# Optimization experiments

Measured on AMD Instinct MI355X. Metric: run time of the kernel, lower is better.

## Reference

```python
import jax, jax.numpy as jnp
import numpy as np
from jax import lax

B, C_IN, T = 64, 40, 8192

def conv1d(x, w, b):
    # x: [B,C,T], w: [O,I,K] (torch Conv1d layout), stride 2, VALID padding
    y = lax.conv_general_dilated(x, w, window_strides=(2,), padding='VALID',
                                 dimension_numbers=('NCH', 'OIH', 'NCH'))
    return y + b[None, :, None]

def avgpool2(x):
    # AvgPool1d(kernel=2, stride=2): pairwise mean, drop trailing odd element
    t2 = x.shape[-1] // 2
    return x[..., :2 * t2].reshape(x.shape[0], x.shape[1], t2, 2).mean(-1)

def setup_inputs():
    key = jax.random.key(0)
    ks = jax.random.split(key, 24)
    def w_init(k, shape, fan_in):
        return jax.random.normal(k, shape, jnp.float32) * (1.0 / np.sqrt(fan_in))
    inp = {}
    inp['x_input'] = jax.random.normal(ks[0], (B, C_IN, T), jnp.float32)
    # per-sample valid lengths in [2048, 8192] so the deep strided stack leaves >=1 frame
    inp['len_mask'] = 2048 + jax.random.randint(ks[1], (B,), 0, T - 2048 + 1, dtype=jnp.int32)
    convs = [(96, C_IN, 10), (96, 96, 5), (96, 96, 5), (96, 96, 5), (96, 96, 5), (96, 96, 5), (128, 96, 3)]
    for i, (o, ci, k) in enumerate(convs):
        inp[f'w{i+1}'] = w_init(ks[2 + 2 * i], (o, ci, k), ci * k)
        inp[f'b{i+1}'] = jnp.zeros((o,), jnp.float32)
    lins = [(128, 128), (64, 128), (5, 64)]
    for i, (o, ci) in enumerate(lins):
        inp[f'lw{i+1}'] = w_init(ks[16 + 2 * i], (o, ci), ci)
        inp[f'lb{i+1}'] = jnp.zeros((o,), jnp.float32)
    return inp

def reference(x_input, len_mask, w1, b1, w2, b2, w3, b3, w4, b4, w5, b5, w6, b6, w7, b7,
              lw1, lb1, lw2, lb2, lw3, lb3):
    # Batched masked equivalent of the per-sample ragged loop: for VALID stride-2 convs,
    # output position j depends only on inputs < valid length when j < valid out-length,
    # so we run batched convs on padded input and track per-sample valid lengths.
    Lv = len_mask.astype(jnp.int32)
    x = jax.nn.relu(conv1d(x_input, w1, b1)); Lv = (Lv - 10) // 2 + 1
    x = jax.nn.relu(conv1d(x, w2, b2));       Lv = (Lv - 5) // 2 + 1
    x = jax.nn.relu(conv1d(x, w3, b3));       Lv = (Lv - 5) // 2 + 1
    # cnn_1d_top (dropout in eval mode = identity)
    x = conv1d(x, w4, b4);        Lv = (Lv - 5) // 2 + 1
    x = jax.nn.relu(avgpool2(x)); Lv = Lv // 2
    x = conv1d(x, w5, b5);        Lv = (Lv - 5) // 2 + 1
    x = jax.nn.relu(avgpool2(x)); Lv = Lv // 2
    x = jax.nn.relu(conv1d(x, w6, b6)); Lv = (Lv - 5) // 2 + 1
    x = jax.nn.relu(conv1d(x, w7, b7)); Lv = (Lv - 3) // 2 + 1
    # AdaptiveMaxPool1d(1) over each sample's valid region
    mask = jnp.arange(x.shape[-1])[None, :] < Lv[:, None]          # [B, T_out]
    x = jnp.max(jnp.where(mask[:, None, :], x, -jnp.inf), axis=-1)  # [B, 128]
    # out1_top MLP head
    h = jax.nn.relu(x @ lw1.T + lb1)
    h = jax.nn.relu(h @ lw2.T + lb2)
    return h @ lw3.T + lb3
```

## Files before the change

### kernel.cpp

```cpp
#include <hip/hip_runtime.h>
#include <hip/hip_bf16.h>
#include <math.h>


typedef __attribute__((ext_vector_type(8))) _Float16 f16x8;
typedef __attribute__((ext_vector_type(4))) float f32x4;

__device__ __forceinline__ unsigned short f2h_bits(float f) {
    union { _Float16 h; unsigned short u; } cv;
    cv.h = (_Float16)f;
    return cv.u;
}

template<int KEFF, int CI, int NBLK, bool IN_FP32, bool RELU, bool OUT_F16, bool POOL>
__global__ __launch_bounds__(512, 2)
void conv_nb(const unsigned short* __restrict__ xh,
             const unsigned short* __restrict__ wpk,
             const float* __restrict__ bias,
             unsigned short* __restrict__ yh,
             float* __restrict__ yf,
             int Tin, int Tout)
{
    constexpr int CO    = 96;
    constexpr int NTHR  = 512;
    constexpr int GTOT  = CI * KEFF;
    constexpr int STEPS = (GTOT + 31) / 32;
    constexpr int RD    = NBLK + KEFF / 2;
    constexpr int NTW   = NBLK / 64;
    constexpr int TOT   = CI * RD;
    constexpr int NIT   = (TOT + NTHR - 1) / NTHR;
    constexpr int PH    = (32 % KEFF == 0) ? 1 : 5;
    constexpr int PERRD = (32 * PH / KEFF) * RD;

    __shared__ unsigned int Bs[TOT];

    const int tid  = threadIdx.x;
    const int lane = tid & 63;
    const int wave = tid >> 6;
    const int mg   = wave & 1;
    const int tg   = wave >> 1;
    const int quad = lane >> 4;
    const int l16  = lane & 15;
    const int wc0  = tg * (NBLK / 4);

    const int nT = (Tout + NBLK - 1) / NBLK;
    const int b  = blockIdx.x / nT;
    const int t0 = (blockIdx.x % nT) * NBLK;

    const float* xf = (const float*)xh;
    const unsigned int* xb = (const unsigned int*)xh + (((size_t)b * CI * Tin) >> 1);
    const int rowd = Tin >> 1;

    #pragma unroll
    for (int it = 0; it < NIT; ++it) {
        int i = tid + it * NTHR;
        if (i < TOT) {
            int r = (unsigned)i / (unsigned)RD, d = i - r * RD;
            unsigned int v;
            if (IN_FP32) {
                int e = 2 * (t0 + d);
                if (e > Tin - 2) e = Tin - 2;
                const float* src = xf + ((size_t)b * CI + r) * Tin + e;
                float2 w = *(const float2*)src;
                v = (unsigned int)f2h_bits(w.x) | ((unsigned int)f2h_bits(w.y) << 16);
            } else {
                int dd = t0 + d;
                if (dd > rowd - 1) dd = rowd - 1;
                v = *(xb + (size_t)r * rowd + dd);
            }
            Bs[i] = v;
        }
    }
    __syncthreads();

    int offb[PH][4];
    #pragma unroll
    for (int ph = 0; ph < PH; ++ph)
        #pragma unroll
        for (int p = 0; p < 4; ++p) {
            int g = 32 * ph + quad * 8 + 2 * p;
            unsigned ci = (unsigned)g / (unsigned)KEFF;
            unsigned dwo = ((unsigned)g - ci * (unsigned)KEFF) >> 1;
            offb[ph][p] = (int)ci * RD + wc0 + l16 + (int)dwo;
        }

    f32x4 acc[3][NTW];
    #pragma unroll
    for (int mt = 0; mt < 3; ++mt)
        #pragma unroll
        for (int nt = 0; nt < NTW; ++nt) acc[mt][nt] = (f32x4)0.f;

    #pragma unroll
    for (int s = 0; s < STEPS; ++s) {
        union BvU { unsigned int u[4]; f16x8 v; } Bv[NTW];
        if (32 * (s + 1) <= GTOT) {
            #pragma unroll
            for (int nt = 0; nt < NTW; ++nt)
                #pragma unroll
                for (int p = 0; p < 4; ++p)
                    Bv[nt].u[p] = Bs[offb[s % PH][p] + (s / PH) * PERRD + nt * 16];
        } else {
            #pragma unroll
            for (int nt = 0; nt < NTW; ++nt)
                #pragma unroll
                for (int p = 0; p < 4; ++p) {
                    int g = 32 * s + quad * 8 + 2 * p;
                    if (g > GTOT - 2) g = GTOT - 2;
                    unsigned ci = (unsigned)g / (unsigned)KEFF;
                    unsigned dwo = ((unsigned)g - ci * (unsigned)KEFF) >> 1;
                    Bv[nt].u[p] = Bs[(int)ci * RD + wc0 + l16 + (int)dwo + nt * 16];
                }
        }

        const unsigned short* ap = wpk + (size_t)s * 6144 + (size_t)(mg * 3) * 512
                                 + (size_t)lane * 8;
        f16x8 Ah[3], Al[3];
        #pragma unroll
        for (int mt = 0; mt < 3; ++mt) {
            Ah[mt] = *(const f16x8*)(ap + mt * 512);
            Al[mt] = *(const f16x8*)(ap + 3072 + mt * 512);
        }
        #pragma unroll
        for (int mt = 0; mt < 3; ++mt)
            #pragma unroll
            for (int nt = 0; nt < NTW; ++nt)
                acc[mt][nt] = __builtin_amdgcn_mfma_f32_16x16x32_f16(Ah[mt], Bv[nt].v, acc[mt][nt], 0, 0, 0);
        #pragma unroll
        for (int mt = 0; mt < 3; ++mt)
            #pragma unroll
            for (int nt = 0; nt < NTW; ++nt)
                acc[mt][nt] = __builtin_amdgcn_mfma_f32_16x16x32_f16(Al[mt], Bv[nt].v, acc[mt][nt], 0, 0, 0);
    }

    #pragma unroll
    for (int mt = 0; mt < 3; ++mt) {
        #pragma unroll
        for (int r = 0; r < 4; ++r) {
            int o = (mg * 3 + mt) * 16 + quad * 4 + r;
            float bv = bias[o];
            #pragma unroll
            for (int nt = 0; nt < NTW; ++nt) {
                int t = t0 + wc0 + nt * 16 + l16;
                float v = acc[mt][nt][r] + bv;
                if (RELU) v = fmaxf(v, 0.f);
                if (POOL) {
                    float sum = v + __shfl_xor(v, 1, 64);
                    if ((lane & 1) == 0 && t + 1 < Tout) {
                        float pr = fmaxf(0.5f * sum, 0.f);
                        size_t pidx = ((size_t)b * CO + o) * (Tout >> 1) + (t >> 1);
                        if (OUT_F16) yh[pidx] = f2h_bits(pr);
                        else         yf[pidx] = pr;
                    }
                } else if (t < Tout) {
                    size_t oidx = ((size_t)b * CO + o) * Tout + t;
                    if (OUT_F16) yh[oidx] = f2h_bits(v);
                    else         yf[oidx] = v;
                }
            }
        }
    }
}

__device__ __forceinline__ void repack_img(const float* __restrict__ w,
                                           unsigned short* __restrict__ wpk,
                                           int idx, int KP, int KW, int CI)
{
    int j = idx & 7, lane = (idx >> 3) & 63, g = idx >> 9;
    int c = g / 24, r = g % 24;
    int mt = r % 6, sh = r / 6;
    int half = sh & 1, s = sh >> 1;
    int S  = c * 2 + s;
    int kg = S * 32 + (lane >> 4) * 8 + j;
    int o  = mt * 16 + (lane & 15);
    int ci = kg / KP, k = kg - ci * KP;
    float val = (ci < CI && k < KW) ? w[((size_t)o * CI + ci) * KW + k] : 0.f;
    _Float16 hh = (_Float16)val;
    union { _Float16 h; unsigned short u; } cv;
    cv.h = (half == 0) ? hh : (_Float16)(val - (float)hh);
    wpk[idx] = cv.u;
}
__device__ __forceinline__ void repack_okc(const float* __restrict__ w,
                                           float* __restrict__ wr,
                                           int idx, int CI, int K, int CO)
{
    int o = idx % CO; int rem = idx / CO; int k = rem % K; int ci = rem / K;
    wr[idx] = w[((size_t)o * CI + ci) * K + k];
}

__global__ void repack_all(const float* w1, const float* w2, const float* w3,
                           const float* w4, const float* w5, const float* w6,
                           const float* w7,
                           unsigned short* p1, unsigned short* p2,
                           unsigned short* p3, unsigned short* p4,
                           unsigned short* p5, float* r6, float* r7)
{
    int idx = blockIdx.x * 256 + threadIdx.x;
    if (idx < 79872)  { repack_img(w1, p1, idx, 10, 10, 40); return; }
    idx -= 79872;
    if (idx < 147456) { repack_img(w2, p2, idx, 8, 5, 96); return; }
    idx -= 147456;
    if (idx < 147456) { repack_img(w3, p3, idx, 8, 5, 96); return; }
    idx -= 147456;
    if (idx < 147456) { repack_img(w4, p4, idx, 8, 5, 96); return; }
    idx -= 147456;
    if (idx < 147456) { repack_img(w5, p5, idx, 8, 5, 96); return; }
    idx -= 147456;
    if (idx < 46080)  { repack_okc(w6, r6, idx, 96, 5, 96); return; }
    idx -= 46080;
    if (idx < 36864)  { repack_okc(w7, r7, idx, 96, 3, 128); return; }
}

__global__ __launch_bounds__(256)
void conv6_k(const float* __restrict__ y5p, const float* __restrict__ w6r,
             const float* __restrict__ b6, float* __restrict__ y6)
{
    __shared__ float s5[96 * 62];
    const int b = blockIdx.x >> 2, ob = blockIdx.x & 3;
    const int tid = threadIdx.x;
    for (int i = tid; i < 96 * 62; i += 256) s5[i] = y5p[(size_t)b * 96 * 62 + i];
    __syncthreads();

    const int wave = __builtin_amdgcn_readfirstlane(tid >> 6);
    const int t = tid & 63;
    if (t < 29) {
        const int o0 = ob * 24 + wave * 6;
        float a[6];
        #pragma unroll
        for (int oo = 0; oo < 6; oo++) a[oo] = 0.f;
        for (int ci = 0; ci < 96; ci++) {
            float xr[5];
            #pragma unroll
            for (int k = 0; k < 5; k++) xr[k] = s5[ci * 62 + 2 * t + k];
            #pragma unroll
            for (int k = 0; k < 5; k++) {
                const float* wp = w6r + (ci * 5 + k) * 96 + o0;
                #pragma unroll
                for (int oo = 0; oo < 6; oo++)
                    a[oo] = fmaf(wp[oo], xr[k], a[oo]);
            }
        }
        #pragma unroll
        for (int oo = 0; oo < 6; oo++)
            y6[((size_t)b * 96 + o0 + oo) * 29 + t] = fmaxf(a[oo] + b6[o0 + oo], 0.f);
    }
}

__global__ __launch_bounds__(256)
void tail2(const float* __restrict__ y6,
           const float* __restrict__ w7r, const float* __restrict__ b7,
           const int* __restrict__ lens,
           const float* __restrict__ lw1, const float* __restrict__ lb1,
           const float* __restrict__ lw2, const float* __restrict__ lb2,
           const float* __restrict__ lw3, const float* __restrict__ lb3,
           float* __restrict__ out)
{
    __shared__ float s6[96 * 29 + 8];
    __shared__ float s7[128 * 14];
    __shared__ float feat[128], h1[128], h2[64];

    const int b = blockIdx.x, tid = threadIdx.x;
    for (int i = tid; i < 96 * 29; i += 256) s6[i] = y6[(size_t)b * 96 * 29 + i];
    __syncthreads();

    const int wave = __builtin_amdgcn_readfirstlane(tid >> 6);
    const int lane = tid & 63;
    const int sub  = lane >> 4;
    const int tl   = lane & 15;
    {
        float a[32];
        #pragma unroll
        for (int oo = 0; oo < 32; oo++) a[oo] = 0.f;
        const int ci0 = sub * 24;
        for (int ci = ci0; ci < ci0 + 24; ci++) {
            float xr[3];
            #pragma unroll
            for (int k = 0; k < 3; k++) xr[k] = s6[ci * 29 + 2 * tl + k];
            #pragma unroll
            for (int k = 0; k < 3; k++) {
                const float* wp = w7r + (ci * 3 + k) * 128 + wave * 32;
                #pragma unroll
                for (int oo = 0; oo < 32; oo++)
                    a[oo] = fmaf(wp[oo], xr[k], a[oo]);
            }
        }
        #pragma unroll
        for (int oo = 0; oo < 32; oo++) {
            float v = a[oo];
            v += __shfl_xor(v, 16, 64);
            v += __shfl_xor(v, 32, 64);
            if (sub == 0 && tl < 14) {
                int o = wave * 32 + oo;
                s7[o * 14 + tl] = fmaxf(v + b7[o], 0.f);
            }
        }
    }
    __syncthreads();

    if (tid < 128) {
        int L = lens[b];
        L = (L - 10) / 2 + 1;
        L = (L - 5) / 2 + 1;
        L = (L - 5) / 2 + 1;
        L = (L - 5) / 2 + 1;
        L = L / 2;
        L = (L - 5) / 2 + 1;
        L = L / 2;
        L = (L - 5) / 2 + 1;
        L = (L - 3) / 2 + 1;
        float m = -INFINITY;
        for (int t = 0; t < L; t++) m = fmaxf(m, s7[tid * 14 + t]);
        feat[tid] = m;
    }
    __syncthreads();

    if (tid < 128) {
        float s = lb1[tid];
        for (int i = 0; i < 128; i++) s = fmaf(lw1[tid * 128 + i], feat[i], s);
        h1[tid] = fmaxf(s, 0.f);
    }
    __syncthreads();
    if (tid < 64) {
        float s = lb2[tid];
        for (int i = 0; i < 128; i++) s = fmaf(lw2[tid * 128 + i], h1[i], s);
        h2[tid] = fmaxf(s, 0.f);
    }
    __syncthreads();
    if (tid < 5) {
        float s = lb3[tid];
        for (int i = 0; i < 64; i++) s = fmaf(lw3[tid * 64 + i], h2[i], s);
        out[b * 5 + tid] = s;
    }
}

extern "C" void kernel_launch(void* const* d_in, const int* in_sizes, int n_in,
                              void* d_out, int out_size, void* d_ws, size_t ws_size,
                              hipStream_t stream)
{
    const float* x    = (const float*)d_in[0];
    const int*   lens = (const int*)  d_in[1];
    const float* w1 = (const float*)d_in[2];   const float* b1 = (const float*)d_in[3];
    const float* w2 = (const float*)d_in[4];   const float* b2 = (const float*)d_in[5];
    const float* w3 = (const float*)d_in[6];   const float* b3 = (const float*)d_in[7];
    const float* w4 = (const float*)d_in[8];   const float* b4 = (const float*)d_in[9];
    const float* w5 = (const float*)d_in[10];  const float* b5 = (const float*)d_in[11];
    const float* w6 = (const float*)d_in[12];  const float* b6 = (const float*)d_in[13];
    const float* w7 = (const float*)d_in[14];  const float* b7 = (const float*)d_in[15];
    const float* lw1 = (const float*)d_in[16]; const float* lb1 = (const float*)d_in[17];
    const float* lw2 = (const float*)d_in[18]; const float* lb2 = (const float*)d_in[19];
    const float* lw3 = (const float*)d_in[20]; const float* lb3 = (const float*)d_in[21];
    float* out = (float*)d_out;
    char*  W   = (char*)d_ws;

    size_t off = 0;
    auto take = [&](size_t bytes) {
        size_t o = off; off = (off + bytes + 255) & ~(size_t)255; return o;
    };
    size_t o_y3h = take(((size_t)64 * 96 * 1020 + 2048) * 2);
    size_t o_y4h = take(((size_t)64 * 96 * 254 + 2048) * 2);
    size_t o_y5p = take((size_t)64 * 96 * 62 * 4 + 1024);
    size_t o_y6  = take((size_t)64 * 96 * 29 * 4);
    size_t o_wp1 = take((size_t)79872 * 2);
    size_t o_wp2 = take((size_t)147456 * 2);
    size_t o_wp3 = take((size_t)147456 * 2);
    size_t o_wp4 = take((size_t)147456 * 2);
    size_t o_wp5 = take((size_t)147456 * 2);
    size_t o_w6r = take((size_t)46080 * 4);
    size_t o_w7r = take((size_t)36864 * 4);
    size_t persist = off;

    auto chunk_bytes = [&](int Bc) -> size_t {
        size_t s = 0;
        s += ((size_t)Bc * 96 * 4092 + 2048) * 2 + 256;
        s += ((size_t)Bc * 96 * 2044 + 2048) * 2 + 256;
        return s;
    };
    int Bc = 64;
    while (Bc > 1 && persist + chunk_bytes(Bc) > ws_size) Bc >>= 1;
    size_t o_y1h = take(((size_t)Bc * 96 * 4092 + 2048) * 2);
    size_t o_y2h = take(((size_t)Bc * 96 * 2044 + 2048) * 2);

    auto US = [&](size_t o) { return (unsigned short*)(W + o); };
    auto FP = [&](size_t o) { return (float*)(W + o); };

    repack_all<<<dim3((752640 + 255) / 256), 256, 0, stream>>>(
        w1, w2, w3, w4, w5, w6, w7,
        US(o_wp1), US(o_wp2), US(o_wp3), US(o_wp4), US(o_wp5),
        FP(o_w6r), FP(o_w7r));

    const int nchunks = 64 / Bc;
    for (int c = 0; c < nchunks; c++) {
        const float* xc = x + (size_t)c * Bc * 40 * 8192;

        conv_nb<10, 40, 256, true, true, true, false><<<dim3(Bc * 16), 512, 0, stream>>>(
            (const unsigned short*)xc, US(o_wp1), b1, US(o_y1h), nullptr, 8192, 4092);
        conv_nb< 8, 96, 128, false, true, true, false><<<dim3(Bc * 16), 512, 0, stream>>>(
            US(o_y1h), US(o_wp2), b2, US(o_y2h), nullptr, 4092, 2044);
        unsigned short* y3h_c = US(o_y3h) + (size_t)c * Bc * 96 * 1020;
        conv_nb< 8, 96, 128, false, true, true, false><<<dim3(Bc * 8), 512, 0, stream>>>(
            US(o_y2h), US(o_wp3), b3, y3h_c, nullptr, 2044, 1020);
    }

    conv_nb<8, 96, 64, false, false, true, true><<<dim3(64 * 8), 512, 0, stream>>>(
        US(o_y3h), US(o_wp4), b4, US(o_y4h), nullptr, 1020, 508);

    conv_nb<8, 96, 64, false, false, false, true><<<dim3(64 * 2), 512, 0, stream>>>(
        US(o_y4h), US(o_wp5), b5, nullptr, FP(o_y5p), 254, 125);

    conv6_k<<<dim3(256), 256, 0, stream>>>(FP(o_y5p), FP(o_w6r), b6, FP(o_y6));

    tail2<<<dim3(64), 256, 0, stream>>>(
        FP(o_y6), FP(o_w7r), b7, lens, lw1, lb1, lw2, lb2, lw3, lb3, out);
}
```

Baseline: 414.1 us.

## Shrink K=5 conv padding to 6, double-buffer MFMA operands, pack f16 stores

The K=5 convolutions now pad the effective kernel to 6 taps instead of 8. This cuts the reduction depth, and with it the MFMA steps and the packed-weight size, by a quarter. A new phase count of 3 handles the new stride. The main loop now prefetches the next step's LDS and weight operands into alternate registers, with sched barriers and setprio around the MFMA block. Non-pooled f16 outputs are paired through a lane shuffle and written as 32-bit stores. Risks are higher register pressure from double buffering, and a possibly dropped last element when Tout is odd in the paired store.

New measurement: 395.9 us. 1.05x faster.

```diff
diff --git a/kernel.cpp b/kernel.cpp
--- a/kernel.cpp
+++ b/kernel.cpp
@@ -29,7 +29,7 @@
     constexpr int NTW   = NBLK / 64;
     constexpr int TOT   = CI * RD;
     constexpr int NIT   = (TOT + NTHR - 1) / NTHR;
-    constexpr int PH    = (32 % KEFF == 0) ? 1 : 5;
+    constexpr int PH    = (32 % KEFF == 0) ? 1 : (((32 * 3) % KEFF == 0) ? 3 : 5);
     constexpr int PERRD = (32 * PH / KEFF) * RD;
 
     __shared__ unsigned int Bs[TOT];
@@ -90,9 +90,9 @@
         #pragma unroll
         for (int nt = 0; nt < NTW; ++nt) acc[mt][nt] = (f32x4)0.f;
 
-    #pragma unroll
-    for (int s = 0; s < STEPS; ++s) {
-        union BvU { unsigned int u[4]; f16x8 v; } Bv[NTW];
+    union BvU { unsigned int u[4]; f16x8 v; };
+
+    auto load_step = [&](int s, BvU (&Bv)[NTW], f16x8 (&Ah)[3], f16x8 (&Al)[3]) {
         if (32 * (s + 1) <= GTOT) {
             #pragma unroll
             for (int nt = 0; nt < NTW; ++nt)
@@ -111,15 +111,15 @@
                     Bv[nt].u[p] = Bs[(int)ci * RD + wc0 + l16 + (int)dwo + nt * 16];
                 }
         }
-
         const unsigned short* ap = wpk + (size_t)s * 6144 + (size_t)(mg * 3) * 512
                                  + (size_t)lane * 8;
-        f16x8 Ah[3], Al[3];
         #pragma unroll
         for (int mt = 0; mt < 3; ++mt) {
             Ah[mt] = *(const f16x8*)(ap + mt * 512);
             Al[mt] = *(const f16x8*)(ap + 3072 + mt * 512);
         }
+    };
+    auto mfma_step = [&](BvU (&Bv)[NTW], f16x8 (&Ah)[3], f16x8 (&Al)[3]) {
         #pragma unroll
         for (int mt = 0; mt < 3; ++mt)
             #pragma unroll
@@ -130,6 +130,24 @@
             #pragma unroll
             for (int nt = 0; nt < NTW; ++nt)
                 acc[mt][nt] = __builtin_amdgcn_mfma_f32_16x16x32_f16(Al[mt], Bv[nt].v, acc[mt][nt], 0, 0, 0);
+    };
+
+    BvU  Bv0[NTW], Bv1[NTW];
+    f16x8 Ah0[3], Al0[3], Ah1[3], Al1[3];
+
+    load_step(0, Bv0, Ah0, Al0);
+    #pragma unroll
+    for (int s = 0; s < STEPS; ++s) {
+        if (s + 1 < STEPS) {
+            if (((s + 1) & 1) == 0) load_step(s + 1, Bv0, Ah0, Al0);
+            else                    load_step(s + 1, Bv1, Ah1, Al1);
+        }
+        __builtin_amdgcn_sched_barrier(0);
+        __builtin_amdgcn_s_setprio(1);
+        if ((s & 1) == 0) mfma_step(Bv0, Ah0, Al0);
+        else              mfma_step(Bv1, Ah1, Al1);
+        __builtin_amdgcn_s_setprio(0);
+        __builtin_amdgcn_sched_barrier(0);
     }
 
     #pragma unroll
@@ -151,10 +169,15 @@
                         if (OUT_F16) yh[pidx] = f2h_bits(pr);
                         else         yf[pidx] = pr;
                     }
+                } else if (OUT_F16) {
+                    unsigned int h = f2h_bits(v);
+                    unsigned int hp = (unsigned int)__shfl_xor((int)h, 1, 64);
+                    if ((lane & 1) == 0 && t + 1 < Tout) {
+                        size_t base = ((size_t)b * CO + o) * Tout + t;
+                        *(unsigned int*)(yh + base) = h | (hp << 16);
+                    }
                 } else if (t < Tout) {
-                    size_t oidx = ((size_t)b * CO + o) * Tout + t;
-                    if (OUT_F16) yh[oidx] = f2h_bits(v);
-                    else         yf[oidx] = v;
+                    yf[((size_t)b * CO + o) * Tout + t] = v;
                 }
             }
         }
@@ -197,14 +220,14 @@
     int idx = blockIdx.x * 256 + threadIdx.x;
     if (idx < 79872)  { repack_img(w1, p1, idx, 10, 10, 40); return; }
     idx -= 79872;
-    if (idx < 147456) { repack_img(w2, p2, idx, 8, 5, 96); return; }
-    idx -= 147456;
-    if (idx < 147456) { repack_img(w3, p3, idx, 8, 5, 96); return; }
-    idx -= 147456;
-    if (idx < 147456) { repack_img(w4, p4, idx, 8, 5, 96); return; }
-    idx -= 147456;
-    if (idx < 147456) { repack_img(w5, p5, idx, 8, 5, 96); return; }
-    idx -= 147456;
+    if (idx < 110592) { repack_img(w2, p2, idx, 6, 5, 96); return; }
+    idx -= 110592;
+    if (idx < 110592) { repack_img(w3, p3, idx, 6, 5, 96); return; }
+    idx -= 110592;
+    if (idx < 110592) { repack_img(w4, p4, idx, 6, 5, 96); return; }
+    idx -= 110592;
+    if (idx < 110592) { repack_img(w5, p5, idx, 6, 5, 96); return; }
+    idx -= 110592;
     if (idx < 46080)  { repack_okc(w6, r6, idx, 96, 5, 96); return; }
     idx -= 46080;
     if (idx < 36864)  { repack_okc(w7, r7, idx, 96, 3, 128); return; }
@@ -360,10 +383,10 @@
     size_t o_y5p = take((size_t)64 * 96 * 62 * 4 + 1024);
     size_t o_y6  = take((size_t)64 * 96 * 29 * 4);
     size_t o_wp1 = take((size_t)79872 * 2);
-    size_t o_wp2 = take((size_t)147456 * 2);
-    size_t o_wp3 = take((size_t)147456 * 2);
-    size_t o_wp4 = take((size_t)147456 * 2);
-    size_t o_wp5 = take((size_t)147456 * 2);
+    size_t o_wp2 = take((size_t)110592 * 2);
+    size_t o_wp3 = take((size_t)110592 * 2);
+    size_t o_wp4 = take((size_t)110592 * 2);
+    size_t o_wp5 = take((size_t)110592 * 2);
     size_t o_w6r = take((size_t)46080 * 4);
     size_t o_w7r = take((size_t)36864 * 4);
     size_t persist = off;
@@ -382,7 +405,7 @@
     auto US = [&](size_t o) { return (unsigned short*)(W + o); };
     auto FP = [&](size_t o) { return (float*)(W + o); };
 
-    repack_all<<<dim3((752640 + 255) / 256), 256, 0, stream>>>(
+    repack_all<<<dim3((605184 + 255) / 256), 256, 0, stream>>>(
         w1, w2, w3, w4, w5, w6, w7,
         US(o_wp1), US(o_wp2), US(o_wp3), US(o_wp4), US(o_wp5),
         FP(o_w6r), FP(o_w7r));
@@ -393,17 +416,17 @@
 
         conv_nb<10, 40, 256, true, true, true, false><<<dim3(Bc * 16), 512, 0, stream>>>(
             (const unsigned short*)xc, US(o_wp1), b1, US(o_y1h), nullptr, 8192, 4092);
-        conv_nb< 8, 96, 128, false, true, true, false><<<dim3(Bc * 16), 512, 0, stream>>>(
+        conv_nb< 6, 96, 128, false, true, true, false><<<dim3(Bc * 16), 512, 0, stream>>>(
             US(o_y1h), US(o_wp2), b2, US(o_y2h), nullptr, 4092, 2044);
         unsigned short* y3h_c = US(o_y3h) + (size_t)c * Bc * 96 * 1020;
-        conv_nb< 8, 96, 128, false, true, true, false><<<dim3(Bc * 8), 512, 0, stream>>>(
+        conv_nb< 6, 96, 128, false, true, true, false><<<dim3(Bc * 8), 512, 0, stream>>>(
             US(o_y2h), US(o_wp3), b3, y3h_c, nullptr, 2044, 1020);
     }
 
-    conv_nb<8, 96, 64, false, false, true, true><<<dim3(64 * 8), 512, 0, stream>>>(
+    conv_nb<6, 96, 64, false, false, true, true><<<dim3(64 * 8), 512, 0, stream>>>(
         US(o_y3h), US(o_wp4), b4, US(o_y4h), nullptr, 1020, 508);
 
-    conv_nb<8, 96, 64, false, false, false, true><<<dim3(64 * 2), 512, 0, stream>>>(
+    conv_nb<6, 96, 64, false, false, false, true><<<dim3(64 * 2), 512, 0, stream>>>(
         US(o_y4h), US(o_wp5), b5, nullptr, FP(o_y5p), 254, 125);
 
     conv6_k<<<dim3(256), 256, 0, stream>>>(FP(o_y5p), FP(o_w6r), b6, FP(o_y6));
```
